# Kernel tuning notes

Hardware: AMD Instinct MI355X
Metric: run time of the kernel (lower is better)

## Reference

```python
import jax, jax.numpy as jnp
import numpy as np

N_NODES = 100000
N_EDGES = 500000
DIM = 128
HID = 128

def setup_inputs() -> dict:
    key = jax.random.key(0)
    k1, k2, k3, k4, k5, k6 = jax.random.split(key, 6)
    z = jax.random.normal(k1, (N_NODES, DIM), dtype=jnp.float32)
    edge_index = jax.random.randint(k2, (2, N_EDGES), 0, N_NODES, dtype=jnp.int64)
    # Linear params (torch default init: U(-1/sqrt(fan_in), 1/sqrt(fan_in)))
    b1_lim = 1.0 / np.sqrt(3 * DIM)
    b2_lim = 1.0 / np.sqrt(HID)
    W1 = jax.random.uniform(k3, (3 * DIM, HID), jnp.float32, -b1_lim, b1_lim)
    b1 = jax.random.uniform(k4, (HID,), jnp.float32, -b1_lim, b1_lim)
    W2 = jax.random.uniform(k5, (HID, 1), jnp.float32, -b2_lim, b2_lim)
    b2 = jax.random.uniform(k6, (1,), jnp.float32, -b2_lim, b2_lim)
    return {"z": z, "edge_index": edge_index, "W1": W1, "b1": b1, "W2": W2, "b2": b2}

def reference(z, edge_index, W1, b1, W2, b2):
    u, v = edge_index[0], edge_index[1]
    zu = z[u]                      # [E, dim]
    zv = z[v]                      # [E, dim]
    feat = jnp.concatenate([zu, zv, jnp.abs(zu - zv)], axis=1)  # [E, 3*dim]
    h = jax.nn.relu(feat @ W1 + b1)   # [E, hid]
    logit = h @ W2 + b2               # [E, 1]
    return logit.squeeze(-1)          # [E]
```

## Files before the change

kernel.cpp:

```cpp
#include <hip/hip_runtime.h>
#include <hip/hip_bf16.h>
#include <cstdint>


typedef __bf16 bf16_t;
typedef __bf16 bf16x8 __attribute__((ext_vector_type(8)));
typedef float  floatx4 __attribute__((ext_vector_type(4)));

#define DIM 128
#define K3 384
#define E_TILE 64
#define ROW_ELEMS 392
#define N_KSTEP 12
#define N_NTILE 8

__device__ inline float bflo(unsigned w) { return __uint_as_float(w << 16); }
__device__ inline float bfhi(unsigned w) { return __uint_as_float(w & 0xffff0000u); }

__global__ void cast_z_kernel(const float* __restrict__ z, bf16_t* __restrict__ zb, int n) {
    int idx = (blockIdx.x * 256 + threadIdx.x) * 8;
    if (idx + 8 > n) return;
    const float4* src = reinterpret_cast<const float4*>(z + idx);
    float4 a = src[0], b = src[1];
    bf16x8 o;
    o[0] = (bf16_t)a.x; o[1] = (bf16_t)a.y; o[2] = (bf16_t)a.z; o[3] = (bf16_t)a.w;
    o[4] = (bf16_t)b.x; o[5] = (bf16_t)b.y; o[6] = (bf16_t)b.z; o[7] = (bf16_t)b.w;
    *reinterpret_cast<bf16x8*>(zb + idx) = o;
}

__global__ void pack_w1_kernel(const float* __restrict__ W1, bf16_t* __restrict__ Wp) {
    int f = blockIdx.x * 256 + threadIdx.x;
    if (f >= N_KSTEP * N_NTILE * 64) return;
    int lane = f & 63;
    int nt   = (f >> 6) & 7;
    int ks   = f >> 9;
    int n  = nt * 16 + (lane & 15);
    int k0 = ks * 32 + (lane >> 4) * 8;
    bf16x8 o;
#pragma unroll
    for (int j = 0; j < 8; ++j) o[j] = (bf16_t)W1[(k0 + j) * DIM + n];
    reinterpret_cast<bf16x8*>(Wp)[f] = o;
}

template <bool PRECAST>
__global__ __launch_bounds__(256)
void decode_kernel(const void* __restrict__ zsrc,
                   const int* __restrict__ ei,
                   const bf16_t* __restrict__ Wp,
                   const float* __restrict__ b1,
                   const float* __restrict__ W2,
                   const float* __restrict__ b2,
                   float* __restrict__ out, int E) {
    __shared__ __align__(16) bf16_t Atile[E_TILE * ROW_ELEMS];
    __shared__ float red[2][E_TILE];

    const int tid = threadIdx.x;
    const int ebase = blockIdx.x * E_TILE;

#pragma unroll
    for (int i = 0; i < 8; ++i) {
        int half  = i * 16 + (tid >> 4);
        int m     = half >> 1;
        int which = half & 1;
        int e = ebase + m; if (e >= E) e = E - 1;
        int node = ei[which * E + e];
        int l16 = tid & 15;
        bf16_t* dst = &Atile[m * ROW_ELEMS + which * DIM + l16 * 8];
        if (PRECAST) {
            const bf16x8* src = reinterpret_cast<const bf16x8*>(
                (const bf16_t*)zsrc + (size_t)node * DIM + l16 * 8);
            *reinterpret_cast<bf16x8*>(dst) = *src;
        } else {
            const float4* src = reinterpret_cast<const float4*>(
                (const float*)zsrc + (size_t)node * DIM + l16 * 8);
            float4 a = src[0], b = src[1];
            bf16x8 o;
            o[0] = (bf16_t)a.x; o[1] = (bf16_t)a.y; o[2] = (bf16_t)a.z; o[3] = (bf16_t)a.w;
            o[4] = (bf16_t)b.x; o[5] = (bf16_t)b.y; o[6] = (bf16_t)b.z; o[7] = (bf16_t)b.w;
            *reinterpret_cast<bf16x8*>(dst) = o;
        }
    }
    __syncthreads();

#pragma unroll
    for (int i = 0; i < 4; ++i) {
        int chunk = i * 256 + tid;
        int m  = chunk >> 4;
        int cc = (chunk & 15) * 8;
        uint4 au = *reinterpret_cast<const uint4*>(&Atile[m * ROW_ELEMS + cc]);
        uint4 av = *reinterpret_cast<const uint4*>(&Atile[m * ROW_ELEMS + DIM + cc]);
        bf16x8 d;
        d[0] = (bf16_t)fabsf(bflo(au.x) - bflo(av.x));
        d[1] = (bf16_t)fabsf(bfhi(au.x) - bfhi(av.x));
        d[2] = (bf16_t)fabsf(bflo(au.y) - bflo(av.y));
        d[3] = (bf16_t)fabsf(bfhi(au.y) - bfhi(av.y));
        d[4] = (bf16_t)fabsf(bflo(au.z) - bflo(av.z));
        d[5] = (bf16_t)fabsf(bfhi(au.z) - bfhi(av.z));
        d[6] = (bf16_t)fabsf(bflo(au.w) - bflo(av.w));
        d[7] = (bf16_t)fabsf(bfhi(au.w) - bfhi(av.w));
        *reinterpret_cast<bf16x8*>(&Atile[m * ROW_ELEMS + 2 * DIM + cc]) = d;
    }
    __syncthreads();

    const int wave = tid >> 6, lane = tid & 63;
    const int wm = wave >> 1, wn = wave & 1;
    const int l15 = lane & 15, quad = lane >> 4;

    floatx4 acc[2][4];
#pragma unroll
    for (int mt = 0; mt < 2; ++mt)
#pragma unroll
        for (int nt = 0; nt < 4; ++nt) acc[mt][nt] = (floatx4)0.0f;

    float b1v[4], w2v[4];
#pragma unroll
    for (int nt = 0; nt < 4; ++nt) {
        int n = (wn * 4 + nt) * 16 + l15;
        b1v[nt] = b1[n];
        w2v[nt] = W2[n];
    }

    const bf16x8* WpF = reinterpret_cast<const bf16x8*>(Wp);
#pragma unroll
    for (int ks = 0; ks < N_KSTEP; ++ks) {
        bf16x8 bfrag[4];
#pragma unroll
        for (int nt = 0; nt < 4; ++nt)
            bfrag[nt] = WpF[(ks * N_NTILE + wn * 4 + nt) * 64 + lane];
#pragma unroll
        for (int mt = 0; mt < 2; ++mt) {
            int m = wm * 32 + mt * 16 + l15;
            bf16x8 afrag = *reinterpret_cast<const bf16x8*>(
                &Atile[m * ROW_ELEMS + ks * 32 + quad * 8]);
#pragma unroll
            for (int nt = 0; nt < 4; ++nt)
                acc[mt][nt] = __builtin_amdgcn_mfma_f32_16x16x32_bf16(
                    afrag, bfrag[nt], acc[mt][nt], 0, 0, 0);
        }
    }

    float partial[2][4];
#pragma unroll
    for (int mt = 0; mt < 2; ++mt)
#pragma unroll
        for (int r = 0; r < 4; ++r) {
            float s = 0.f;
#pragma unroll
            for (int nt = 0; nt < 4; ++nt) {
                float h = acc[mt][nt][r] + b1v[nt];
                h = fmaxf(h, 0.f);
                s += h * w2v[nt];
            }
            s += __shfl_xor(s, 1);
            s += __shfl_xor(s, 2);
            s += __shfl_xor(s, 4);
            s += __shfl_xor(s, 8);
            partial[mt][r] = s;
        }
    if (l15 == 0) {
#pragma unroll
        for (int mt = 0; mt < 2; ++mt)
#pragma unroll
            for (int r = 0; r < 4; ++r) {
                int m = wm * 32 + mt * 16 + quad * 4 + r;
                red[wn][m] = partial[mt][r];
            }
    }
    __syncthreads();

    if (tid < E_TILE) {
        int e = ebase + tid;
        if (e < E) out[e] = red[0][tid] + red[1][tid] + b2[0];
    }
}

extern "C" void kernel_launch(void* const* d_in, const int* in_sizes, int n_in,
                              void* d_out, int out_size, void* d_ws, size_t ws_size,
                              hipStream_t stream) {
    const float* z  = (const float*)d_in[0];
    const int*   ei = (const int*)d_in[1];
    const float* W1 = (const float*)d_in[2];
    const float* b1 = (const float*)d_in[3];
    const float* W2 = (const float*)d_in[4];
    const float* b2 = (const float*)d_in[5];
    float* out = (float*)d_out;

    const int E  = in_sizes[1] / 2;
    const int zn = in_sizes[0];

    const size_t zb_bytes = (size_t)zn * sizeof(bf16_t);
    const size_t wp_bytes = (size_t)N_KSTEP * N_NTILE * 64 * 16;
    const bool precast = ws_size >= zb_bytes + wp_bytes;

    bf16_t* zb = (bf16_t*)d_ws;
    bf16_t* wp = precast ? (bf16_t*)((char*)d_ws + zb_bytes) : (bf16_t*)d_ws;

    hipLaunchKernelGGL(pack_w1_kernel, dim3((N_KSTEP * N_NTILE * 64 + 255) / 256),
                       dim3(256), 0, stream, W1, wp);

    const int nblocks = (E + E_TILE - 1) / E_TILE;
    if (precast) {
        hipLaunchKernelGGL(cast_z_kernel, dim3((zn / 8 + 255) / 256), dim3(256),
                           0, stream, z, zb, zn);
        hipLaunchKernelGGL((decode_kernel<true>), dim3(nblocks), dim3(256), 0,
                           stream, (const void*)zb, ei, wp, b1, W2, b2, out, E);
    } else {
        hipLaunchKernelGGL((decode_kernel<false>), dim3(nblocks), dim3(256), 0,
                           stream, (const void*)z, ei, wp, b1, W2, b2, out, E);
    }
}
```

Baseline: 182.6 us.

## Precompute per-node W1 projections and gather them per edge instead of full GEMM

Splits feat@W1 algebraically: the zu and zv blocks of W1 are applied once per node (100k nodes) in a precompute kernel that also casts z to bf16 and packs the |zu-zv| weight block. The edge kernel gathers the per-node projections plus bf16 z rows, sums the projections, and runs only the K=128 |zu-zv| GEMM per edge. This cuts per-edge MFMA work by two thirds. In exchange it adds a node-level GEMM, a 256-wide bf16 projection table to write and gather, and extra bf16 rounding of the partial sums.

After: 205.9 us. 1.13x slower.

```diff
diff --git a/kernel.cpp b/kernel.cpp
--- a/kernel.cpp
+++ b/kernel.cpp
@@ -8,25 +8,219 @@
 typedef float  floatx4 __attribute__((ext_vector_type(4)));
 
 #define DIM 128
+#define LDA 136
+#define NB_TILE 64
+#define E_TILE 64
+#define PACK_BLOCKS 8
+
+__device__ inline float bflo(unsigned w) { return __uint_as_float(w << 16); }
+__device__ inline float bfhi(unsigned w) { return __uint_as_float(w & 0xffff0000u); }
+__device__ inline float bf2f(unsigned short u) { return __uint_as_float(((unsigned)u) << 16); }
+
+__global__ __launch_bounds__(256)
+void precompute_kernel(const float* __restrict__ z,
+                       const float* __restrict__ W1,
+                       bf16_t* __restrict__ zb,
+                       bf16_t* __restrict__ P,
+                       bf16_t* __restrict__ Wc,
+                       int Nn, int nblk) {
+    __shared__ __align__(16) bf16_t A[NB_TILE * LDA];
+    const int tid = threadIdx.x;
+
+    if ((int)blockIdx.x >= nblk) {
+        int pid = ((int)blockIdx.x - nblk) * 256 + tid;
+        int lane = pid & 63;
+        int fidx = pid >> 6;
+        int nt = fidx & 7, ks = fidx >> 3;
+        int n  = nt * 16 + (lane & 15);
+        int k0 = ks * 32 + (lane >> 4) * 8;
+        bf16x8 o;
+#pragma unroll
+        for (int j = 0; j < 8; ++j) o[j] = (bf16_t)W1[(256 + k0 + j) * DIM + n];
+        reinterpret_cast<bf16x8*>(Wc)[fidx * 64 + lane] = o;
+        return;
+    }
+
+    const int node0 = (int)blockIdx.x * NB_TILE;
+#pragma unroll
+    for (int i = 0; i < 4; ++i) {
+        int t = i * 256 + tid;
+        int m = t >> 4, c = (t & 15) * 8;
+        int node = node0 + m;
+        int nc = node < Nn ? node : Nn - 1;
+        const float4* src = reinterpret_cast<const float4*>(z + (size_t)nc * DIM + c);
+        float4 a = src[0], b = src[1];
+        bf16x8 o;
+        o[0]=(bf16_t)a.x; o[1]=(bf16_t)a.y; o[2]=(bf16_t)a.z; o[3]=(bf16_t)a.w;
+        o[4]=(bf16_t)b.x; o[5]=(bf16_t)b.y; o[6]=(bf16_t)b.z; o[7]=(bf16_t)b.w;
+        *reinterpret_cast<bf16x8*>(&A[m * LDA + c]) = o;
+        if (node < Nn)
+            *reinterpret_cast<bf16x8*>(zb + (size_t)node * DIM + c) = o;
+    }
+    __syncthreads();
+
+    const int wave = tid >> 6, lane = tid & 63;
+    const int l15 = lane & 15, quad = lane >> 4;
+
+    floatx4 acc[4][4];
+#pragma unroll
+    for (int mt = 0; mt < 4; ++mt)
+#pragma unroll
+        for (int nt = 0; nt < 4; ++nt) acc[mt][nt] = (floatx4)0.0f;
+
+#pragma unroll
+    for (int ks = 0; ks < 4; ++ks) {
+        bf16x8 bfrag[4];
+#pragma unroll
+        for (int nt = 0; nt < 4; ++nt) {
+            int np = wave * 64 + nt * 16 + l15;
+            int k0 = ks * 32 + quad * 8;
+            const float* wsrc = (np < DIM) ? &W1[(size_t)k0 * DIM + np]
+                                           : &W1[(size_t)(DIM + k0) * DIM + (np - DIM)];
+#pragma unroll
+            for (int j = 0; j < 8; ++j) bfrag[nt][j] = (bf16_t)wsrc[(size_t)j * DIM];
+        }
+#pragma unroll
+        for (int mt = 0; mt < 4; ++mt) {
+            bf16x8 afrag = *reinterpret_cast<const bf16x8*>(
+                &A[(mt * 16 + l15) * LDA + ks * 32 + quad * 8]);
+#pragma unroll
+            for (int nt = 0; nt < 4; ++nt)
+                acc[mt][nt] = __builtin_amdgcn_mfma_f32_16x16x32_bf16(
+                    afrag, bfrag[nt], acc[mt][nt], 0, 0, 0);
+        }
+    }
+
+#pragma unroll
+    for (int mt = 0; mt < 4; ++mt)
+#pragma unroll
+        for (int r = 0; r < 4; ++r) {
+            int node = node0 + mt * 16 + quad * 4 + r;
+            if (node < Nn) {
+#pragma unroll
+                for (int nt = 0; nt < 4; ++nt) {
+                    int np = wave * 64 + nt * 16 + l15;
+                    P[(size_t)node * 256 + np] = (bf16_t)acc[mt][nt][r];
+                }
+            }
+        }
+}
+
+__global__ __launch_bounds__(256)
+void edge_kernel(const bf16_t* __restrict__ zb,
+                 const bf16_t* __restrict__ P,
+                 const bf16_t* __restrict__ Wc,
+                 const int* __restrict__ ei,
+                 const float* __restrict__ b1,
+                 const float* __restrict__ W2,
+                 const float* __restrict__ b2,
+                 float* __restrict__ out, int E) {
+    __shared__ __align__(16) bf16_t A[E_TILE * LDA];
+    __shared__ __align__(16) bf16_t H[E_TILE * LDA];
+    __shared__ float red[4][E_TILE];
+
+    const int tid = threadIdx.x;
+    const int ebase = (int)blockIdx.x * E_TILE;
+
+#pragma unroll
+    for (int i = 0; i < 4; ++i) {
+        int t = i * 256 + tid;
+        int m = t >> 4, c = (t & 15) * 8;
+        int e = ebase + m; if (e >= E) e = E - 1;
+        int u = ei[e], v = ei[E + e];
+        uint4 zu = *reinterpret_cast<const uint4*>(zb + (size_t)u * DIM + c);
+        uint4 zv = *reinterpret_cast<const uint4*>(zb + (size_t)v * DIM + c);
+        uint4 pa = *reinterpret_cast<const uint4*>(P + (size_t)u * 256 + c);
+        uint4 pb = *reinterpret_cast<const uint4*>(P + (size_t)v * 256 + DIM + c);
+        bf16x8 d, h;
+        d[0]=(bf16_t)fabsf(bflo(zu.x)-bflo(zv.x));
+        d[1]=(bf16_t)fabsf(bfhi(zu.x)-bfhi(zv.x));
+        d[2]=(bf16_t)fabsf(bflo(zu.y)-bflo(zv.y));
+        d[3]=(bf16_t)fabsf(bfhi(zu.y)-bfhi(zv.y));
+        d[4]=(bf16_t)fabsf(bflo(zu.z)-bflo(zv.z));
+        d[5]=(bf16_t)fabsf(bfhi(zu.z)-bfhi(zv.z));
+        d[6]=(bf16_t)fabsf(bflo(zu.w)-bflo(zv.w));
+        d[7]=(bf16_t)fabsf(bfhi(zu.w)-bfhi(zv.w));
+        h[0]=(bf16_t)(bflo(pa.x)+bflo(pb.x));
+        h[1]=(bf16_t)(bfhi(pa.x)+bfhi(pb.x));
+        h[2]=(bf16_t)(bflo(pa.y)+bflo(pb.y));
+        h[3]=(bf16_t)(bfhi(pa.y)+bfhi(pb.y));
+        h[4]=(bf16_t)(bflo(pa.z)+bflo(pb.z));
+        h[5]=(bf16_t)(bfhi(pa.z)+bfhi(pb.z));
+        h[6]=(bf16_t)(bflo(pa.w)+bflo(pb.w));
+        h[7]=(bf16_t)(bfhi(pa.w)+bfhi(pb.w));
+        *reinterpret_cast<bf16x8*>(&A[m * LDA + c]) = d;
+        *reinterpret_cast<bf16x8*>(&H[m * LDA + c]) = h;
+    }
+    __syncthreads();
+
+    const int wave = tid >> 6, lane = tid & 63;
+    const int l15 = lane & 15, quad = lane >> 4;
+
+    float b1v[2], w2v[2];
+#pragma unroll
+    for (int nt = 0; nt < 2; ++nt) {
+        int n = (wave * 2 + nt) * 16 + l15;
+        b1v[nt] = b1[n];
+        w2v[nt] = W2[n];
+    }
+
+    floatx4 acc[4][2];
+#pragma unroll
+    for (int mt = 0; mt < 4; ++mt)
+#pragma unroll
+        for (int nt = 0; nt < 2; ++nt) acc[mt][nt] = (floatx4)0.0f;
+
+    const bf16x8* WcF = reinterpret_cast<const bf16x8*>(Wc);
+#pragma unroll
+    for (int ks = 0; ks < 4; ++ks) {
+        bf16x8 bfrag[2];
+#pragma unroll
+        for (int nt = 0; nt < 2; ++nt)
+            bfrag[nt] = WcF[(ks * 8 + wave * 2 + nt) * 64 + lane];
+#pragma unroll
+        for (int mt = 0; mt < 4; ++mt) {
+            bf16x8 afrag = *reinterpret_cast<const bf16x8*>(
+                &A[(mt * 16 + l15) * LDA + ks * 32 + quad * 8]);
+#pragma unroll
+            for (int nt = 0; nt < 2; ++nt)
+                acc[mt][nt] = __builtin_amdgcn_mfma_f32_16x16x32_bf16(
+                    afrag, bfrag[nt], acc[mt][nt], 0, 0, 0);
+        }
+    }
+
+    const unsigned short* Hs = reinterpret_cast<const unsigned short*>(H);
+#pragma unroll
+    for (int mt = 0; mt < 4; ++mt)
+#pragma unroll
+        for (int r = 0; r < 4; ++r) {
+            int m = mt * 16 + quad * 4 + r;
+            float s = 0.f;
+#pragma unroll
+            for (int nt = 0; nt < 2; ++nt) {
+                int n = (wave * 2 + nt) * 16 + l15;
+                float h = acc[mt][nt][r] + b1v[nt] + bf2f(Hs[m * LDA + n]);
+                h = fmaxf(h, 0.f);
+                s += h * w2v[nt];
+            }
+            s += __shfl_xor(s, 1);
+            s += __shfl_xor(s, 2);
+            s += __shfl_xor(s, 4);
+            s += __shfl_xor(s, 8);
+            if (l15 == 0) red[wave][m] = s;
+        }
+    __syncthreads();
+
+    if (tid < E_TILE) {
+        int e = ebase + tid;
+        if (e < E) out[e] = red[0][tid] + red[1][tid] + red[2][tid] + red[3][tid] + b2[0];
+    }
+}
+
 #define K3 384
-#define E_TILE 64
 #define ROW_ELEMS 392
 #define N_KSTEP 12
 #define N_NTILE 8
-
-__device__ inline float bflo(unsigned w) { return __uint_as_float(w << 16); }
-__device__ inline float bfhi(unsigned w) { return __uint_as_float(w & 0xffff0000u); }
-
-__global__ void cast_z_kernel(const float* __restrict__ z, bf16_t* __restrict__ zb, int n) {
-    int idx = (blockIdx.x * 256 + threadIdx.x) * 8;
-    if (idx + 8 > n) return;
-    const float4* src = reinterpret_cast<const float4*>(z + idx);
-    float4 a = src[0], b = src[1];
-    bf16x8 o;
-    o[0] = (bf16_t)a.x; o[1] = (bf16_t)a.y; o[2] = (bf16_t)a.z; o[3] = (bf16_t)a.w;
-    o[4] = (bf16_t)b.x; o[5] = (bf16_t)b.y; o[6] = (bf16_t)b.z; o[7] = (bf16_t)b.w;
-    *reinterpret_cast<bf16x8*>(zb + idx) = o;
-}
 
 __global__ void pack_w1_kernel(const float* __restrict__ W1, bf16_t* __restrict__ Wp) {
     int f = blockIdx.x * 256 + threadIdx.x;
@@ -42,21 +236,18 @@
     reinterpret_cast<bf16x8*>(Wp)[f] = o;
 }
 
-template <bool PRECAST>
 __global__ __launch_bounds__(256)
-void decode_kernel(const void* __restrict__ zsrc,
-                   const int* __restrict__ ei,
-                   const bf16_t* __restrict__ Wp,
-                   const float* __restrict__ b1,
-                   const float* __restrict__ W2,
-                   const float* __restrict__ b2,
-                   float* __restrict__ out, int E) {
+void decode_fallback(const float* __restrict__ zsrc,
+                     const int* __restrict__ ei,
+                     const bf16_t* __restrict__ Wp,
+                     const float* __restrict__ b1,
+                     const float* __restrict__ W2,
+                     const float* __restrict__ b2,
+                     float* __restrict__ out, int E) {
     __shared__ __align__(16) bf16_t Atile[E_TILE * ROW_ELEMS];
     __shared__ float red[2][E_TILE];
-
     const int tid = threadIdx.x;
     const int ebase = blockIdx.x * E_TILE;
-
 #pragma unroll
     for (int i = 0; i < 8; ++i) {
         int half  = i * 16 + (tid >> 4);
@@ -66,22 +257,15 @@
         int node = ei[which * E + e];
         int l16 = tid & 15;
         bf16_t* dst = &Atile[m * ROW_ELEMS + which * DIM + l16 * 8];
-        if (PRECAST) {
-            const bf16x8* src = reinterpret_cast<const bf16x8*>(
-                (const bf16_t*)zsrc + (size_t)node * DIM + l16 * 8);
-            *reinterpret_cast<bf16x8*>(dst) = *src;
-        } else {
-            const float4* src = reinterpret_cast<const float4*>(
-                (const float*)zsrc + (size_t)node * DIM + l16 * 8);
-            float4 a = src[0], b = src[1];
-            bf16x8 o;
-            o[0] = (bf16_t)a.x; o[1] = (bf16_t)a.y; o[2] = (bf16_t)a.z; o[3] = (bf16_t)a.w;
-            o[4] = (bf16_t)b.x; o[5] = (bf16_t)b.y; o[6] = (bf16_t)b.z; o[7] = (bf16_t)b.w;
-            *reinterpret_cast<bf16x8*>(dst) = o;
-        }
-    }
-    __syncthreads();
-
+        const float4* src = reinterpret_cast<const float4*>(
+            zsrc + (size_t)node * DIM + l16 * 8);
+        float4 a = src[0], b = src[1];
+        bf16x8 o;
+        o[0]=(bf16_t)a.x; o[1]=(bf16_t)a.y; o[2]=(bf16_t)a.z; o[3]=(bf16_t)a.w;
+        o[4]=(bf16_t)b.x; o[5]=(bf16_t)b.y; o[6]=(bf16_t)b.z; o[7]=(bf16_t)b.w;
+        *reinterpret_cast<bf16x8*>(dst) = o;
+    }
+    __syncthreads();
 #pragma unroll
     for (int i = 0; i < 4; ++i) {
         int chunk = i * 256 + tid;
@@ -90,28 +274,25 @@
         uint4 au = *reinterpret_cast<const uint4*>(&Atile[m * ROW_ELEMS + cc]);
         uint4 av = *reinterpret_cast<const uint4*>(&Atile[m * ROW_ELEMS + DIM + cc]);
         bf16x8 d;
-        d[0] = (bf16_t)fabsf(bflo(au.x) - bflo(av.x));
-        d[1] = (bf16_t)fabsf(bfhi(au.x) - bfhi(av.x));
-        d[2] = (bf16_t)fabsf(bflo(au.y) - bflo(av.y));
-        d[3] = (bf16_t)fabsf(bfhi(au.y) - bfhi(av.y));
-        d[4] = (bf16_t)fabsf(bflo(au.z) - bflo(av.z));
-        d[5] = (bf16_t)fabsf(bfhi(au.z) - bfhi(av.z));
-        d[6] = (bf16_t)fabsf(bflo(au.w) - bflo(av.w));
-        d[7] = (bf16_t)fabsf(bfhi(au.w) - bfhi(av.w));
+        d[0]=(bf16_t)fabsf(bflo(au.x)-bflo(av.x));
+        d[1]=(bf16_t)fabsf(bfhi(au.x)-bfhi(av.x));
+        d[2]=(bf16_t)fabsf(bflo(au.y)-bflo(av.y));
+        d[3]=(bf16_t)fabsf(bfhi(au.y)-bfhi(av.y));
+        d[4]=(bf16_t)fabsf(bflo(au.z)-bflo(av.z));
+        d[5]=(bf16_t)fabsf(bfhi(au.z)-bfhi(av.z));
+        d[6]=(bf16_t)fabsf(bflo(au.w)-bflo(av.w));
+        d[7]=(bf16_t)fabsf(bfhi(au.w)-bfhi(av.w));
         *reinterpret_cast<bf16x8*>(&Atile[m * ROW_ELEMS + 2 * DIM + cc]) = d;
     }
     __syncthreads();
-
     const int wave = tid >> 6, lane = tid & 63;
     const int wm = wave >> 1, wn = wave & 1;
     const int l15 = lane & 15, quad = lane >> 4;
-
     floatx4 acc[2][4];
 #pragma unroll
     for (int mt = 0; mt < 2; ++mt)
 #pragma unroll
         for (int nt = 0; nt < 4; ++nt) acc[mt][nt] = (floatx4)0.0f;
-
     float b1v[4], w2v[4];
 #pragma unroll
     for (int nt = 0; nt < 4; ++nt) {
@@ -119,7 +300,6 @@
         b1v[nt] = b1[n];
         w2v[nt] = W2[n];
     }
-
     const bf16x8* WpF = reinterpret_cast<const bf16x8*>(Wp);
 #pragma unroll
     for (int ks = 0; ks < N_KSTEP; ++ks) {
@@ -138,7 +318,6 @@
                     afrag, bfrag[nt], acc[mt][nt], 0, 0, 0);
         }
     }
-
     float partial[2][4];
 #pragma unroll
     for (int mt = 0; mt < 2; ++mt)
@@ -167,7 +346,6 @@
             }
     }
     __syncthreads();
-
     if (tid < E_TILE) {
         int e = ebase + tid;
         if (e < E) out[e] = red[0][tid] + red[1][tid] + b2[0];
@@ -186,26 +364,28 @@
     float* out = (float*)d_out;
 
     const int E  = in_sizes[1] / 2;
-    const int zn = in_sizes[0];
-
-    const size_t zb_bytes = (size_t)zn * sizeof(bf16_t);
-    const size_t wp_bytes = (size_t)N_KSTEP * N_NTILE * 64 * 16;
-    const bool precast = ws_size >= zb_bytes + wp_bytes;
-
-    bf16_t* zb = (bf16_t*)d_ws;
-    bf16_t* wp = precast ? (bf16_t*)((char*)d_ws + zb_bytes) : (bf16_t*)d_ws;
-
-    hipLaunchKernelGGL(pack_w1_kernel, dim3((N_KSTEP * N_NTILE * 64 + 255) / 256),
-                       dim3(256), 0, stream, W1, wp);
-
-    const int nblocks = (E + E_TILE - 1) / E_TILE;
-    if (precast) {
-        hipLaunchKernelGGL(cast_z_kernel, dim3((zn / 8 + 255) / 256), dim3(256),
-                           0, stream, z, zb, zn);
-        hipLaunchKernelGGL((decode_kernel<true>), dim3(nblocks), dim3(256), 0,
-                           stream, (const void*)zb, ei, wp, b1, W2, b2, out, E);
+    const int Nn = in_sizes[0] / DIM;
+
+    const size_t zb_bytes = (size_t)Nn * DIM * sizeof(bf16_t);
+    const size_t p_bytes  = (size_t)Nn * 256 * sizeof(bf16_t);
+    const size_t wc_bytes = 4 * 8 * 64 * 16;
+
+    const int eblocks = (E + E_TILE - 1) / E_TILE;
+
+    if (ws_size >= zb_bytes + p_bytes + wc_bytes) {
+        bf16_t* zb = (bf16_t*)d_ws;
+        bf16_t* P  = (bf16_t*)((char*)d_ws + zb_bytes);
+        bf16_t* Wc = (bf16_t*)((char*)d_ws + zb_bytes + p_bytes);
+        const int nblk = (Nn + NB_TILE - 1) / NB_TILE;
+        hipLaunchKernelGGL(precompute_kernel, dim3(nblk + PACK_BLOCKS), dim3(256),
+                           0, stream, z, W1, zb, P, Wc, Nn, nblk);
+        hipLaunchKernelGGL(edge_kernel, dim3(eblocks), dim3(256), 0, stream,
+                           zb, P, Wc, ei, b1, W2, b2, out, E);
     } else {
-        hipLaunchKernelGGL((decode_kernel<false>), dim3(nblocks), dim3(256), 0,
-                           stream, (const void*)z, ei, wp, b1, W2, b2, out, E);
-    }
-}
+        bf16_t* wp = (bf16_t*)d_ws;
+        hipLaunchKernelGGL(pack_w1_kernel, dim3((N_KSTEP * N_NTILE * 64 + 255) / 256),
+                           dim3(256), 0, stream, W1, wp);
+        hipLaunchKernelGGL(decode_fallback, dim3(eblocks), dim3(256), 0, stream,
+                           z, ei, wp, b1, W2, b2, out, E);
+    }
+}
```

## Merge prep kernels and shrink edge tile to 32 with per-wave N split

Applied to the files above, without the earlier changes.

Folds W1 packing and the z bf16 cast into one prep kernel, removing one launch. The main edge kernel now handles 32 edges per block instead of 64. The four waves split the 128 hidden columns four ways, and each thread issues four 16-byte gathers of one node row back to back. A launch-bounds occupancy hint is added. Smaller tiles and LDS use should give more resident blocks and more gathers in flight, but each block loads W1 fragments for half as many edges, which doubles total W1 traffic.

New measurement: 187.1 us. +2.5%, slower.

```diff
diff --git a/kernel.cpp b/kernel.cpp
--- a/kernel.cpp
+++ b/kernel.cpp
@@ -8,55 +8,171 @@
 typedef float  floatx4 __attribute__((ext_vector_type(4)));
 
 #define DIM 128
-#define K3 384
-#define E_TILE 64
-#define ROW_ELEMS 392
+#define LDA3 392
+#define ET 32
 #define N_KSTEP 12
 #define N_NTILE 8
+#define PACKBLK 24
 
 __device__ inline float bflo(unsigned w) { return __uint_as_float(w << 16); }
 __device__ inline float bfhi(unsigned w) { return __uint_as_float(w & 0xffff0000u); }
 
-__global__ void cast_z_kernel(const float* __restrict__ z, bf16_t* __restrict__ zb, int n) {
-    int idx = (blockIdx.x * 256 + threadIdx.x) * 8;
-    if (idx + 8 > n) return;
+__global__ __launch_bounds__(256)
+void prep_kernel(const float* __restrict__ z, const float* __restrict__ W1,
+                 bf16_t* __restrict__ zb, bf16_t* __restrict__ Wp, int nelem) {
+    const int tid = threadIdx.x;
+    if ((int)blockIdx.x < PACKBLK) {
+        int f = (int)blockIdx.x * 256 + tid;
+        int lane = f & 63;
+        int nt   = (f >> 6) & 7;
+        int ks   = f >> 9;
+        int n  = nt * 16 + (lane & 15);
+        int k0 = ks * 32 + (lane >> 4) * 8;
+        bf16x8 o;
+#pragma unroll
+        for (int j = 0; j < 8; ++j) o[j] = (bf16_t)W1[(k0 + j) * DIM + n];
+        reinterpret_cast<bf16x8*>(Wp)[f] = o;
+        return;
+    }
+    int idx = (((int)blockIdx.x - PACKBLK) * 256 + tid) * 8;
+    if (idx + 8 > nelem) return;
     const float4* src = reinterpret_cast<const float4*>(z + idx);
     float4 a = src[0], b = src[1];
     bf16x8 o;
-    o[0] = (bf16_t)a.x; o[1] = (bf16_t)a.y; o[2] = (bf16_t)a.z; o[3] = (bf16_t)a.w;
-    o[4] = (bf16_t)b.x; o[5] = (bf16_t)b.y; o[6] = (bf16_t)b.z; o[7] = (bf16_t)b.w;
+    o[0]=(bf16_t)a.x; o[1]=(bf16_t)a.y; o[2]=(bf16_t)a.z; o[3]=(bf16_t)a.w;
+    o[4]=(bf16_t)b.x; o[5]=(bf16_t)b.y; o[6]=(bf16_t)b.z; o[7]=(bf16_t)b.w;
     *reinterpret_cast<bf16x8*>(zb + idx) = o;
 }
 
-__global__ void pack_w1_kernel(const float* __restrict__ W1, bf16_t* __restrict__ Wp) {
-    int f = blockIdx.x * 256 + threadIdx.x;
-    if (f >= N_KSTEP * N_NTILE * 64) return;
-    int lane = f & 63;
-    int nt   = (f >> 6) & 7;
-    int ks   = f >> 9;
-    int n  = nt * 16 + (lane & 15);
-    int k0 = ks * 32 + (lane >> 4) * 8;
-    bf16x8 o;
-#pragma unroll
-    for (int j = 0; j < 8; ++j) o[j] = (bf16_t)W1[(k0 + j) * DIM + n];
-    reinterpret_cast<bf16x8*>(Wp)[f] = o;
+__global__ __launch_bounds__(256, 4)
+void edge_kernel(const bf16_t* __restrict__ zb,
+                 const bf16_t* __restrict__ Wp,
+                 const int* __restrict__ ei,
+                 const float* __restrict__ b1,
+                 const float* __restrict__ W2,
+                 const float* __restrict__ b2,
+                 float* __restrict__ out, int E) {
+    __shared__ __align__(16) bf16_t A[ET * LDA3];
+    __shared__ float red[4][ET];
+
+    const int tid = threadIdx.x;
+    const int ebase = (int)blockIdx.x * ET;
+    const int el  = tid >> 3;
+    const int sub = tid & 7;
+    const int which = sub >> 2;
+    const int chunk = sub & 3;
+
+    int e = ebase + el; if (e >= E) e = E - 1;
+    int node = ei[which * E + e];
+
+    const uint4* p = reinterpret_cast<const uint4*>(
+        zb + (size_t)node * DIM + chunk * 32);
+    uint4 g[4];
+#pragma unroll
+    for (int j = 0; j < 4; ++j) g[j] = p[j];
+
+    const int wave = tid >> 6, lane = tid & 63;
+    const int l15 = lane & 15, quad = lane >> 4;
+
+    float b1v[2], w2v[2];
+#pragma unroll
+    for (int nt = 0; nt < 2; ++nt) {
+        int n = (wave * 2 + nt) * 16 + l15;
+        b1v[nt] = b1[n];
+        w2v[nt] = W2[n];
+    }
+
+    bf16_t* dst = &A[el * LDA3 + which * DIM + chunk * 32];
+#pragma unroll
+    for (int j = 0; j < 4; ++j)
+        *reinterpret_cast<uint4*>(dst + j * 8) = g[j];
+    __syncthreads();
+
+#pragma unroll
+    for (int i = 0; i < 2; ++i) {
+        int idx = i * 256 + tid;
+        int m  = idx >> 4;
+        int cc = (idx & 15) * 8;
+        uint4 au = *reinterpret_cast<const uint4*>(&A[m * LDA3 + cc]);
+        uint4 av = *reinterpret_cast<const uint4*>(&A[m * LDA3 + DIM + cc]);
+        bf16x8 d;
+        d[0]=(bf16_t)fabsf(bflo(au.x)-bflo(av.x));
+        d[1]=(bf16_t)fabsf(bfhi(au.x)-bfhi(av.x));
+        d[2]=(bf16_t)fabsf(bflo(au.y)-bflo(av.y));
+        d[3]=(bf16_t)fabsf(bfhi(au.y)-bfhi(av.y));
+        d[4]=(bf16_t)fabsf(bflo(au.z)-bflo(av.z));
+        d[5]=(bf16_t)fabsf(bfhi(au.z)-bfhi(av.z));
+        d[6]=(bf16_t)fabsf(bflo(au.w)-bflo(av.w));
+        d[7]=(bf16_t)fabsf(bfhi(au.w)-bfhi(av.w));
+        *reinterpret_cast<bf16x8*>(&A[m * LDA3 + 2 * DIM + cc]) = d;
+    }
+    __syncthreads();
+
+    floatx4 acc[2][2];
+#pragma unroll
+    for (int mt = 0; mt < 2; ++mt)
+#pragma unroll
+        for (int nt = 0; nt < 2; ++nt) acc[mt][nt] = (floatx4)0.0f;
+
+    const bf16x8* WpF = reinterpret_cast<const bf16x8*>(Wp);
+#pragma unroll
+    for (int ks = 0; ks < N_KSTEP; ++ks) {
+        bf16x8 bfrag[2];
+#pragma unroll
+        for (int nt = 0; nt < 2; ++nt)
+            bfrag[nt] = WpF[(ks * N_NTILE + wave * 2 + nt) * 64 + lane];
+#pragma unroll
+        for (int mt = 0; mt < 2; ++mt) {
+            bf16x8 afrag = *reinterpret_cast<const bf16x8*>(
+                &A[(mt * 16 + l15) * LDA3 + ks * 32 + quad * 8]);
+#pragma unroll
+            for (int nt = 0; nt < 2; ++nt)
+                acc[mt][nt] = __builtin_amdgcn_mfma_f32_16x16x32_bf16(
+                    afrag, bfrag[nt], acc[mt][nt], 0, 0, 0);
+        }
+    }
+
+#pragma unroll
+    for (int mt = 0; mt < 2; ++mt)
+#pragma unroll
+        for (int r = 0; r < 4; ++r) {
+            int m = mt * 16 + quad * 4 + r;
+            float s = 0.f;
+#pragma unroll
+            for (int nt = 0; nt < 2; ++nt) {
+                float h = acc[mt][nt][r] + b1v[nt];
+                h = fmaxf(h, 0.f);
+                s += h * w2v[nt];
+            }
+            s += __shfl_xor(s, 1);
+            s += __shfl_xor(s, 2);
+            s += __shfl_xor(s, 4);
+            s += __shfl_xor(s, 8);
+            if (l15 == 0) red[wave][m] = s;
+        }
+    __syncthreads();
+
+    if (tid < ET) {
+        int eo = ebase + tid;
+        if (eo < E) out[eo] = red[0][tid] + red[1][tid] + red[2][tid] + red[3][tid] + b2[0];
+    }
 }
 
-template <bool PRECAST>
+#define E_TILE 64
+#define ROW_ELEMS 392
+
 __global__ __launch_bounds__(256)
-void decode_kernel(const void* __restrict__ zsrc,
-                   const int* __restrict__ ei,
-                   const bf16_t* __restrict__ Wp,
-                   const float* __restrict__ b1,
-                   const float* __restrict__ W2,
-                   const float* __restrict__ b2,
-                   float* __restrict__ out, int E) {
+void decode_fallback(const float* __restrict__ zsrc,
+                     const int* __restrict__ ei,
+                     const bf16_t* __restrict__ Wp,
+                     const float* __restrict__ b1,
+                     const float* __restrict__ W2,
+                     const float* __restrict__ b2,
+                     float* __restrict__ out, int E) {
     __shared__ __align__(16) bf16_t Atile[E_TILE * ROW_ELEMS];
     __shared__ float red[2][E_TILE];
-
     const int tid = threadIdx.x;
     const int ebase = blockIdx.x * E_TILE;
-
 #pragma unroll
     for (int i = 0; i < 8; ++i) {
         int half  = i * 16 + (tid >> 4);
@@ -66,22 +182,15 @@
         int node = ei[which * E + e];
         int l16 = tid & 15;
         bf16_t* dst = &Atile[m * ROW_ELEMS + which * DIM + l16 * 8];
-        if (PRECAST) {
-            const bf16x8* src = reinterpret_cast<const bf16x8*>(
-                (const bf16_t*)zsrc + (size_t)node * DIM + l16 * 8);
-            *reinterpret_cast<bf16x8*>(dst) = *src;
-        } else {
-            const float4* src = reinterpret_cast<const float4*>(
-                (const float*)zsrc + (size_t)node * DIM + l16 * 8);
-            float4 a = src[0], b = src[1];
-            bf16x8 o;
-            o[0] = (bf16_t)a.x; o[1] = (bf16_t)a.y; o[2] = (bf16_t)a.z; o[3] = (bf16_t)a.w;
-            o[4] = (bf16_t)b.x; o[5] = (bf16_t)b.y; o[6] = (bf16_t)b.z; o[7] = (bf16_t)b.w;
-            *reinterpret_cast<bf16x8*>(dst) = o;
-        }
-    }
-    __syncthreads();
-
+        const float4* src = reinterpret_cast<const float4*>(
+            zsrc + (size_t)node * DIM + l16 * 8);
+        float4 a = src[0], b = src[1];
+        bf16x8 o;
+        o[0]=(bf16_t)a.x; o[1]=(bf16_t)a.y; o[2]=(bf16_t)a.z; o[3]=(bf16_t)a.w;
+        o[4]=(bf16_t)b.x; o[5]=(bf16_t)b.y; o[6]=(bf16_t)b.z; o[7]=(bf16_t)b.w;
+        *reinterpret_cast<bf16x8*>(dst) = o;
+    }
+    __syncthreads();
 #pragma unroll
     for (int i = 0; i < 4; ++i) {
         int chunk = i * 256 + tid;
@@ -90,28 +199,25 @@
         uint4 au = *reinterpret_cast<const uint4*>(&Atile[m * ROW_ELEMS + cc]);
         uint4 av = *reinterpret_cast<const uint4*>(&Atile[m * ROW_ELEMS + DIM + cc]);
         bf16x8 d;
-        d[0] = (bf16_t)fabsf(bflo(au.x) - bflo(av.x));
-        d[1] = (bf16_t)fabsf(bfhi(au.x) - bfhi(av.x));
-        d[2] = (bf16_t)fabsf(bflo(au.y) - bflo(av.y));
-        d[3] = (bf16_t)fabsf(bfhi(au.y) - bfhi(av.y));
-        d[4] = (bf16_t)fabsf(bflo(au.z) - bflo(av.z));
-        d[5] = (bf16_t)fabsf(bfhi(au.z) - bfhi(av.z));
-        d[6] = (bf16_t)fabsf(bflo(au.w) - bflo(av.w));
-        d[7] = (bf16_t)fabsf(bfhi(au.w) - bfhi(av.w));
+        d[0]=(bf16_t)fabsf(bflo(au.x)-bflo(av.x));
+        d[1]=(bf16_t)fabsf(bfhi(au.x)-bfhi(av.x));
+        d[2]=(bf16_t)fabsf(bflo(au.y)-bflo(av.y));
+        d[3]=(bf16_t)fabsf(bfhi(au.y)-bfhi(av.y));
+        d[4]=(bf16_t)fabsf(bflo(au.z)-bflo(av.z));
+        d[5]=(bf16_t)fabsf(bfhi(au.z)-bfhi(av.z));
+        d[6]=(bf16_t)fabsf(bflo(au.w)-bflo(av.w));
+        d[7]=(bf16_t)fabsf(bfhi(au.w)-bfhi(av.w));
         *reinterpret_cast<bf16x8*>(&Atile[m * ROW_ELEMS + 2 * DIM + cc]) = d;
     }
     __syncthreads();
-
     const int wave = tid >> 6, lane = tid & 63;
     const int wm = wave >> 1, wn = wave & 1;
     const int l15 = lane & 15, quad = lane >> 4;
-
     floatx4 acc[2][4];
 #pragma unroll
     for (int mt = 0; mt < 2; ++mt)
 #pragma unroll
         for (int nt = 0; nt < 4; ++nt) acc[mt][nt] = (floatx4)0.0f;
-
     float b1v[4], w2v[4];
 #pragma unroll
     for (int nt = 0; nt < 4; ++nt) {
@@ -119,7 +225,6 @@
         b1v[nt] = b1[n];
         w2v[nt] = W2[n];
     }
-
     const bf16x8* WpF = reinterpret_cast<const bf16x8*>(Wp);
 #pragma unroll
     for (int ks = 0; ks < N_KSTEP; ++ks) {
@@ -138,7 +243,6 @@
                     afrag, bfrag[nt], acc[mt][nt], 0, 0, 0);
         }
     }
-
     float partial[2][4];
 #pragma unroll
     for (int mt = 0; mt < 2; ++mt)
@@ -167,7 +271,6 @@
             }
     }
     __syncthreads();
-
     if (tid < E_TILE) {
         int e = ebase + tid;
         if (e < E) out[e] = red[0][tid] + red[1][tid] + b2[0];
@@ -185,27 +288,27 @@
     const float* b2 = (const float*)d_in[5];
     float* out = (float*)d_out;
 
-    const int E  = in_sizes[1] / 2;
-    const int zn = in_sizes[0];
-
-    const size_t zb_bytes = (size_t)zn * sizeof(bf16_t);
+    const int E     = in_sizes[1] / 2;
+    const int nelem = in_sizes[0];
+
     const size_t wp_bytes = (size_t)N_KSTEP * N_NTILE * 64 * 16;
-    const bool precast = ws_size >= zb_bytes + wp_bytes;
-
-    bf16_t* zb = (bf16_t*)d_ws;
-    bf16_t* wp = precast ? (bf16_t*)((char*)d_ws + zb_bytes) : (bf16_t*)d_ws;
-
-    hipLaunchKernelGGL(pack_w1_kernel, dim3((N_KSTEP * N_NTILE * 64 + 255) / 256),
-                       dim3(256), 0, stream, W1, wp);
-
-    const int nblocks = (E + E_TILE - 1) / E_TILE;
-    if (precast) {
-        hipLaunchKernelGGL(cast_z_kernel, dim3((zn / 8 + 255) / 256), dim3(256),
-                           0, stream, z, zb, zn);
-        hipLaunchKernelGGL((decode_kernel<true>), dim3(nblocks), dim3(256), 0,
-                           stream, (const void*)zb, ei, wp, b1, W2, b2, out, E);
+    const size_t zb_bytes = (size_t)nelem * sizeof(bf16_t);
+
+    bf16_t* wp = (bf16_t*)d_ws;
+
+    if (ws_size >= wp_bytes + zb_bytes) {
+        bf16_t* zbuf = (bf16_t*)((char*)d_ws + wp_bytes);
+        const int castblk = (nelem / 8 + 255) / 256;
+        hipLaunchKernelGGL(prep_kernel, dim3(PACKBLK + castblk), dim3(256),
+                           0, stream, z, W1, zbuf, wp, nelem);
+        const int eblocks = (E + ET - 1) / ET;
+        hipLaunchKernelGGL(edge_kernel, dim3(eblocks), dim3(256), 0, stream,
+                           zbuf, wp, ei, b1, W2, b2, out, E);
     } else {
-        hipLaunchKernelGGL((decode_kernel<false>), dim3(nblocks), dim3(256), 0,
-                           stream, (const void*)z, ei, wp, b1, W2, b2, out, E);
+        hipLaunchKernelGGL(prep_kernel, dim3(PACKBLK), dim3(256),
+                           0, stream, z, W1, (bf16_t*)nullptr, wp, 0);
+        const int eblocks = (E + E_TILE - 1) / E_TILE;
+        hipLaunchKernelGGL(decode_fallback, dim3(eblocks), dim3(256), 0, stream,
+                           z, ei, wp, b1, W2, b2, out, E);
     }
 }
```
